# Kernel tuning notes

Measured on AMD Instinct MI355X. Metric: run time of the kernel, lower is better.

Reference implementation:

```python
import jax, jax.numpy as jnp
import numpy as np

N_USER, N_ITEM, N_BUNDLE = 200000, 100000, 50000
EMBED_DIM = 128
B, L = 8192, 100  # batch of bundles, max items per bundle


def setup_inputs() -> dict:
    key = jax.random.key(0)
    ks = jax.random.split(key, 12)
    d, d2 = EMBED_DIM, 2 * EMBED_DIM
    x_u = jax.random.randint(ks[0], (B,), 0, N_USER)
    x_b = jax.random.randint(ks[1], (B,), 0, N_BUNDLE)
    items = jax.random.randint(ks[2], (B, L), 0, N_ITEM)
    # ragged bundle sizes in [10, L]; padded+masked form of the CSR gather
    lengths = jax.random.randint(ks[3], (B,), 10, L + 1)
    mask = jnp.arange(L)[None, :] < lengths[:, None]  # [B, L] bool
    return {
        "x_u": x_u,
        "x_b": x_b,
        "items": items,
        "mask": mask,
        "emb_u": jax.random.normal(ks[4], (N_USER, d), jnp.float32) * 0.1,
        "emb_i": jax.random.normal(ks[5], (N_ITEM, d), jnp.float32) * 0.1,
        "emb_b": jax.random.normal(ks[6], (N_BUNDLE, d), jnp.float32) * 0.1,
        "A": jax.random.normal(ks[7], (N_ITEM, d), jnp.float32) * 0.1,
        "fc1_w": jax.random.normal(ks[8], (d2, d2), jnp.float32) / np.sqrt(d2),
        "fc1_b": jnp.zeros((d2,), jnp.float32),
        "fc2_w": jax.random.normal(ks[9], (d2, d2), jnp.float32) / np.sqrt(d2),
        "fc2_b": jnp.zeros((d2,), jnp.float32),
        "out_w": jax.random.normal(ks[10], (1, d2), jnp.float32) / np.sqrt(d2),
        "out_b": jnp.zeros((1,), jnp.float32),
    }


def reference(x_u, x_b, items, mask, emb_u, emb_i, emb_b, A,
              fc1_w, fc1_b, fc2_w, fc2_b, out_w, out_b):
    # DAM.forward_bundle with the attention() per-bundle loop vectorized
    h_u = emb_u[x_u]                       # [B, d]
    h_b = emb_b[x_b]                       # [B, d]
    item_e = emb_i[items]                  # [B, L, d] ragged gather (padded)
    a_e = A[items]                         # [B, L, d]
    # w = softmax_l( sum_d e_u * A[item] ) per bundle, over valid items only
    scores = jnp.einsum('bd,bld->bl', h_u, a_e)
    scores = jnp.where(mask, scores, -jnp.inf)
    w = jax.nn.softmax(scores, axis=1)     # [B, L]
    h_x = jnp.einsum('bl,bld->bd', w, item_e)
    h = jnp.concatenate([h_u, h_b + h_x], axis=1)   # [B, 2d]
    h = jax.nn.leaky_relu(h @ fc1_w.T + fc1_b)
    h = jax.nn.leaky_relu(h @ fc2_w.T + fc2_b)
    return h @ out_w.T + out_b             # [B, 1]
```

## Files before the change

### kernel.cpp

```cpp
#include <hip/hip_runtime.h>
#include <hip/hip_bf16.h>

#define D   128
#define D2  256
#define H1P 272

typedef short bf16x8 __attribute__((ext_vector_type(8)));
typedef float f32x4  __attribute__((ext_vector_type(4)));

__device__ __forceinline__ float bf2f(unsigned short u) {
    return __uint_as_float(((unsigned int)u) << 16);
}
__device__ __forceinline__ float bflo(unsigned int p) { return __uint_as_float(p << 16); }
__device__ __forceinline__ float bfhi(unsigned int p) { return __uint_as_float(p & 0xffff0000u); }
__device__ __forceinline__ unsigned short f2bf(float f) {
    __hip_bfloat16 h = __float2bfloat16(f);
    return *(unsigned short*)&h;
}

template<bool BF>
__device__ __forceinline__ float ld1(const void* p, size_t i) {
    if constexpr (BF) return bf2f(((const unsigned short*)p)[i]);
    else              return ((const float*)p)[i];
}

template<bool BF>
__device__ __forceinline__ void load8f(const void* p, size_t elem_off, float* r) {
    if constexpr (BF) {
        uint4 v = *(const uint4*)((const unsigned short*)p + elem_off);
        r[0]=bflo(v.x); r[1]=bfhi(v.x); r[2]=bflo(v.y); r[3]=bfhi(v.y);
        r[4]=bflo(v.z); r[5]=bfhi(v.z); r[6]=bflo(v.w); r[7]=bfhi(v.w);
    } else {
        const float4* q = (const float4*)((const float*)p + elem_off);
        float4 a = q[0], b = q[1];
        r[0]=a.x; r[1]=a.y; r[2]=a.z; r[3]=a.w;
        r[4]=b.x; r[5]=b.y; r[6]=b.z; r[7]=b.w;
    }
}

__device__ __forceinline__ bool probe_is_bf16(const unsigned int* probe) {
    const int lane = threadIdx.x & 63;
    int cnt = 0;
    #pragma unroll
    for (int i = 0; i < 4; ++i) {
        unsigned int e = (probe[lane + 64 * i] >> 7) & 0xffu;
        cnt += (e >= 90 && e < 130) ? 1 : 0;
    }
    #pragma unroll
    for (int o = 32; o; o >>= 1) cnt += __shfl_xor(cnt, o);
    return cnt >= 128;
}

template<bool BF>
__device__ __forceinline__ void attn_body(
    const int* __restrict__ x_u, const int* __restrict__ x_b,
    const int* __restrict__ items, const void* __restrict__ mask, int mmode,
    const void* __restrict__ emb_u, const void* __restrict__ emb_i,
    const void* __restrict__ emb_b, const void* __restrict__ Aw,
    unsigned short* __restrict__ h_out, int L,
    float* hu_s, float* w_s, int* it_s, int* cnt_s, float* reds_s,
    float (*part_s)[132])
{
    const int b  = blockIdx.x;
    const int t  = threadIdx.x;
    const int wv = t >> 6, ln = t & 63;

    const int xu = x_u[b], xb = x_b[b];
    float hu = 0.f;
    if (t < D) { hu = ld1<BF>(emb_u, (size_t)xu * D + t); hu_s[t] = hu; }

    bool valid = false;
    if (t < 128) {
        const int tc = (t < L) ? t : (L - 1);
        it_s[t] = items[(size_t)b * L + tc];
        if (t < L) {
            const size_t mi = (size_t)b * L + t;
            if (mmode == 0)      valid = ((const int*)mask)[mi] != 0;
            else if (mmode == 1) valid = ((const unsigned char*)mask)[mi] != 0;
            else                 valid = ((const unsigned short*)mask)[mi] != 0;
        }
    }
    unsigned long long bm = __ballot(valid);
    if (ln == 0) cnt_s[wv] = __popcll(bm);
    __syncthreads();
    const int len = cnt_s[0] + cnt_s[1] + cnt_s[2] + cnt_s[3];

    const int g = t >> 4, m16 = t & 15;

    uint4 pre0[3], pre1[3];
    if constexpr (BF) {
        const unsigned short* EI = (const unsigned short*)emb_i;
        #pragma unroll
        for (int i = 0; i < 3; ++i) {
            const int l0 = 32 * i + g, l1 = 32 * i + 16 + g;
            const int i0 = (l0 < len) ? it_s[l0] : it_s[0];
            const int i1 = (l1 < len) ? it_s[l1] : it_s[0];
            pre0[i] = *(const uint4*)(EI + (size_t)i0 * D + 8 * m16);
            pre1[i] = *(const uint4*)(EI + (size_t)i1 * D + 8 * m16);
        }
    }

    const int item = t >> 1, half = t & 1;
    float e = 0.f;
    if (item < len) {
        float acc = 0.f, r[8];
        const size_t base = (size_t)it_s[item] * D + half * 64;
        const float4* hu4 = (const float4*)hu_s + half * 16;
        #pragma unroll
        for (int c = 0; c < 8; ++c) {
            load8f<BF>(Aw, base + 8 * c, r);
            float4 ha = hu4[2 * c], hb2 = hu4[2 * c + 1];
            acc += ha.x * r[0] + ha.y * r[1] + ha.z * r[2] + ha.w * r[3]
                 + hb2.x * r[4] + hb2.y * r[5] + hb2.z * r[6] + hb2.w * r[7];
        }
        acc += __shfl_xor(acc, 1);
        e = __expf(acc);
    }
    if (half == 0) w_s[item] = e;
    float es = (half == 0) ? e : 0.f;
    #pragma unroll
    for (int o = 32; o; o >>= 1) es += __shfl_xor(es, o);
    if (ln == 0) reds_s[wv] = es;
    __syncthreads();
    const float sm  = reds_s[0] + reds_s[1] + reds_s[2] + reds_s[3];
    const float inv = (sm > 0.f) ? 1.f / sm : 0.f;

    float acc8[8];
    #pragma unroll
    for (int k = 0; k < 8; ++k) acc8[k] = 0.f;
    if constexpr (BF) {
        #pragma unroll
        for (int i = 0; i < 3; ++i) {
            const float w0 = w_s[32 * i + g], w1 = w_s[32 * i + 16 + g];
            const uint4 p0 = pre0[i], p1 = pre1[i];
            acc8[0] += w0 * bflo(p0.x) + w1 * bflo(p1.x);
            acc8[1] += w0 * bfhi(p0.x) + w1 * bfhi(p1.x);
            acc8[2] += w0 * bflo(p0.y) + w1 * bflo(p1.y);
            acc8[3] += w0 * bfhi(p0.y) + w1 * bfhi(p1.y);
            acc8[4] += w0 * bflo(p0.z) + w1 * bflo(p1.z);
            acc8[5] += w0 * bfhi(p0.z) + w1 * bfhi(p1.z);
            acc8[6] += w0 * bflo(p0.w) + w1 * bflo(p1.w);
            acc8[7] += w0 * bfhi(p0.w) + w1 * bfhi(p1.w);
        }
        if (len > 96) {
            const int l0 = 96 + g;
            const int i0 = (l0 < len) ? it_s[l0] : it_s[0];
            const float w0 = w_s[l0];
            const uint4 p0 = *(const uint4*)((const unsigned short*)emb_i
                                             + (size_t)i0 * D + 8 * m16);
            acc8[0] += w0 * bflo(p0.x); acc8[1] += w0 * bfhi(p0.x);
            acc8[2] += w0 * bflo(p0.y); acc8[3] += w0 * bfhi(p0.y);
            acc8[4] += w0 * bflo(p0.z); acc8[5] += w0 * bfhi(p0.z);
            acc8[6] += w0 * bflo(p0.w); acc8[7] += w0 * bfhi(p0.w);
        }
    } else {
        const int nit = (len + 31) & ~31;
        for (int i = 0; i < nit; i += 32) {
            const int l0 = i + g, l1 = i + 16 + g;
            const int i0 = (l0 < len) ? it_s[l0] : it_s[0];
            const int i1 = (l1 < len) ? it_s[l1] : it_s[0];
            const float w0 = w_s[l0], w1 = w_s[l1];
            float r0[8], r1[8];
            load8f<false>(emb_i, (size_t)i0 * D + 8 * m16, r0);
            load8f<false>(emb_i, (size_t)i1 * D + 8 * m16, r1);
            #pragma unroll
            for (int k = 0; k < 8; ++k) acc8[k] += w0 * r0[k] + w1 * r1[k];
        }
    }
    f32x4 v0 = {acc8[0] * inv, acc8[1] * inv, acc8[2] * inv, acc8[3] * inv};
    f32x4 v1 = {acc8[4] * inv, acc8[5] * inv, acc8[6] * inv, acc8[7] * inv};
    *(f32x4*)&part_s[g][8 * m16]     = v0;
    *(f32x4*)&part_s[g][8 * m16 + 4] = v1;
    __syncthreads();

    if (t < D) {
        float hx = 0.f;
        #pragma unroll
        for (int gg = 0; gg < 16; ++gg) hx += part_s[gg][t];
        const float hbv = ld1<BF>(emb_b, (size_t)xb * D + t);
        h_out[(size_t)b * D2 + t]     = f2bf(hu);
        h_out[(size_t)b * D2 + D + t] = f2bf(hbv + hx);
    }
}

__global__ __launch_bounds__(256) void attn_kernel(
    const int* x_u, const int* x_b, const int* items, const void* mask,
    const void* emb_u, const void* emb_i, const void* emb_b, const void* A,
    unsigned short* h_out, int L)
{
    __shared__ float hu_s[D];
    __shared__ float w_s[128];
    __shared__ int   it_s[128];
    __shared__ int   cnt_s[4];
    __shared__ float reds_s[4];
    __shared__ float part_s[16][132];

    const bool bf = probe_is_bf16((const unsigned int*)emb_u);
    const unsigned char* mb = (const unsigned char*)mask;
    const int mm = (mb[1] == 0) ? 0 : ((mb[0] == 1) ? 1 : 2);

    if (bf) attn_body<true >(x_u, x_b, items, mask, mm, emb_u, emb_i, emb_b, A,
                             h_out, L, hu_s, w_s, it_s, cnt_s, reds_s, part_s);
    else    attn_body<false>(x_u, x_b, items, mask, mm, emb_u, emb_i, emb_b, A,
                             h_out, L, hu_s, w_s, it_s, cnt_s, reds_s, part_s);
}

template<bool BF>
__device__ __forceinline__ bf16x8 load_w8(const void* W, size_t off) {
    if constexpr (BF) {
        return *(const bf16x8*)((const unsigned short*)W + off);
    } else {
        const float* p = (const float*)W + off;
        float4 a = *(const float4*)p;
        float4 b = *(const float4*)(p + 4);
        bf16x8 r;
        r[0] = (short)f2bf(a.x); r[1] = (short)f2bf(a.y);
        r[2] = (short)f2bf(a.z); r[3] = (short)f2bf(a.w);
        r[4] = (short)f2bf(b.x); r[5] = (short)f2bf(b.y);
        r[6] = (short)f2bf(b.z); r[7] = (short)f2bf(b.w);
        return r;
    }
}

template<bool BF>
__device__ __forceinline__ void mlp_body(
    const unsigned short* __restrict__ X,
    const void* __restrict__ fc1_w, const void* __restrict__ fc1_b,
    const void* __restrict__ fc2_w, const void* __restrict__ fc2_b,
    const void* __restrict__ out_w, const void* __restrict__ out_b,
    void* __restrict__ out,
    unsigned short* h1_s, float (*po_s)[16])
{
    const int tid  = threadIdx.x;
    const int wave = tid >> 6;
    const int lane = tid & 63;
    const int l16  = lane & 15;
    const int quad = lane >> 4;
    const int mt   = blockIdx.x * 16;

    bf16x8 afrag[8];
    const size_t abase = (size_t)(mt + l16) * D2 + quad * 8;
    #pragma unroll
    for (int kc = 0; kc < 8; ++kc)
        afrag[kc] = *(const bf16x8*)(X + abase + kc * 32);

    #pragma unroll
    for (int jj = 0; jj < 4; ++jj) {
        const int jt = wave * 4 + jj;
        const size_t bbase = (size_t)(jt * 16 + l16) * D2 + quad * 8;
        f32x4 acc = {0.f, 0.f, 0.f, 0.f};
        #pragma unroll
        for (int kc = 0; kc < 8; ++kc) {
            bf16x8 bfrag = load_w8<BF>(fc1_w, bbase + kc * 32);
            acc = __builtin_amdgcn_mfma_f32_16x16x32_bf16(afrag[kc], bfrag, acc, 0, 0, 0);
        }
        const int j  = jt * 16 + l16;
        const float bj = ld1<BF>(fc1_b, j);
        #pragma unroll
        for (int r = 0; r < 4; ++r) {
            float v = acc[r] + bj;
            v = v > 0.f ? v : 0.01f * v;
            h1_s[(quad * 4 + r) * H1P + j] = f2bf(v);
        }
    }
    __syncthreads();

    bf16x8 afrag2[8];
    #pragma unroll
    for (int kc = 0; kc < 8; ++kc)
        afrag2[kc] = *(const bf16x8*)&h1_s[l16 * H1P + quad * 8 + kc * 32];

    float po[4] = {0.f, 0.f, 0.f, 0.f};
    #pragma unroll
    for (int jj = 0; jj < 4; ++jj) {
        const int jt = wave * 4 + jj;
        const size_t bbase = (size_t)(jt * 16 + l16) * D2 + quad * 8;
        f32x4 acc = {0.f, 0.f, 0.f, 0.f};
        #pragma unroll
        for (int kc = 0; kc < 8; ++kc) {
            bf16x8 bfrag = load_w8<BF>(fc2_w, bbase + kc * 32);
            acc = __builtin_amdgcn_mfma_f32_16x16x32_bf16(afrag2[kc], bfrag, acc, 0, 0, 0);
        }
        const int j  = jt * 16 + l16;
        const float bj = ld1<BF>(fc2_b, j);
        const float wj = ld1<BF>(out_w, j);
        #pragma unroll
        for (int r = 0; r < 4; ++r) {
            float v = acc[r] + bj;
            v = v > 0.f ? v : 0.01f * v;
            po[r] += v * wj;
        }
    }
    #pragma unroll
    for (int r = 0; r < 4; ++r) {
        #pragma unroll
        for (int o = 1; o < 16; o <<= 1) po[r] += __shfl_xor(po[r], o);
    }
    if (l16 == 0) {
        #pragma unroll
        for (int r = 0; r < 4; ++r) po_s[wave][quad * 4 + r] = po[r];
    }
    __syncthreads();

    if (tid < 16) {
        const float v = po_s[0][tid] + po_s[1][tid] + po_s[2][tid] + po_s[3][tid]
                      + ld1<BF>(out_b, 0);
        if constexpr (BF) ((unsigned short*)out)[mt + tid] = f2bf(v);
        else              ((float*)out)[mt + tid] = v;
    }
}

__global__ __launch_bounds__(256) void mlp_kernel(
    const unsigned short* X,
    const void* fc1_w, const void* fc1_b, const void* fc2_w, const void* fc2_b,
    const void* out_w, const void* out_b, void* out, const void* probe)
{
    __shared__ unsigned short h1_s[16 * H1P];
    __shared__ float po_s[4][16];

    const bool bf = probe_is_bf16((const unsigned int*)probe);
    if (bf) mlp_body<true >(X, fc1_w, fc1_b, fc2_w, fc2_b, out_w, out_b, out, h1_s, po_s);
    else    mlp_body<false>(X, fc1_w, fc1_b, fc2_w, fc2_b, out_w, out_b, out, h1_s, po_s);
}

extern "C" void kernel_launch(void* const* d_in, const int* in_sizes, int n_in,
                              void* d_out, int out_size, void* d_ws, size_t ws_size,
                              hipStream_t stream) {
    const int*  x_u   = (const int*)d_in[0];
    const int*  x_b   = (const int*)d_in[1];
    const int*  items = (const int*)d_in[2];
    const void* mask  = d_in[3];
    const void* emb_u = d_in[4];
    const void* emb_i = d_in[5];
    const void* emb_b = d_in[6];
    const void* A     = d_in[7];
    const void* fc1_w = d_in[8];
    const void* fc1_b = d_in[9];
    const void* fc2_w = d_in[10];
    const void* fc2_b = d_in[11];
    const void* out_w = d_in[12];
    const void* out_b = d_in[13];

    const int B = in_sizes[0];
    const int L = in_sizes[2] / B;

    unsigned short* h = (unsigned short*)d_ws;

    attn_kernel<<<B, 256, 0, stream>>>(x_u, x_b, items, mask,
                                       emb_u, emb_i, emb_b, A, h, L);
    mlp_kernel<<<B / 16, 256, 0, stream>>>(h, fc1_w, fc1_b, fc2_w, fc2_b,
                                           out_w, out_b, d_out, emb_u);
}
```

Before: 320.7 us.

## Map one bundle per wavefront in attention kernel, replacing shared memory with shuffles

The attention kernel now assigns each bundle to a single 64-lane wavefront instead of a 256-thread block. Item ids, weights and partial sums move between lanes with shuffles instead of shared memory and __syncthreads. This removes block-level barriers and LDS traffic and lets each wave proceed on its own. In exchange, each wave issues all the gathers for its bundle serially, with less memory-level parallelism per bundle, and carries more register pressure (hu[32], e[7]). It also assumes L <= 128 and B divisible by 4.

```diff
diff --git a/kernel.cpp b/kernel.cpp
--- a/kernel.cpp
+++ b/kernel.cpp
@@ -38,6 +38,19 @@
     }
 }
 
+__device__ __forceinline__ void store8bf(unsigned short* p, const float* r) {
+    union { unsigned short u[8]; uint4 v; } pk;
+    #pragma unroll
+    for (int k = 0; k < 8; ++k) pk.u[k] = f2bf(r[k]);
+    *(uint4*)p = pk.v;
+}
+
+__device__ __forceinline__ bool read_mask(const void* mask, int mmode, size_t i) {
+    if (mmode == 0) return ((const int*)mask)[i] != 0;
+    if (mmode == 1) return ((const unsigned char*)mask)[i] != 0;
+    return ((const unsigned short*)mask)[i] != 0;
+}
+
 __device__ __forceinline__ bool probe_is_bf16(const unsigned int* probe) {
     const int lane = threadIdx.x & 63;
     int cnt = 0;
@@ -52,134 +65,103 @@
 }
 
 template<bool BF>
-__device__ __forceinline__ void attn_body(
+__device__ __forceinline__ void attn_wave(
     const int* __restrict__ x_u, const int* __restrict__ x_b,
     const int* __restrict__ items, const void* __restrict__ mask, int mmode,
     const void* __restrict__ emb_u, const void* __restrict__ emb_i,
     const void* __restrict__ emb_b, const void* __restrict__ Aw,
-    unsigned short* __restrict__ h_out, int L,
-    float* hu_s, float* w_s, int* it_s, int* cnt_s, float* reds_s,
-    float (*part_s)[132])
+    unsigned short* __restrict__ h_out, int L)
 {
-    const int b  = blockIdx.x;
-    const int t  = threadIdx.x;
-    const int wv = t >> 6, ln = t & 63;
+    const int lane = threadIdx.x & 63;
+    const int wv   = threadIdx.x >> 6;
+    const int b    = blockIdx.x * 4 + wv;
 
     const int xu = x_u[b], xb = x_b[b];
-    float hu = 0.f;
-    if (t < D) { hu = ld1<BF>(emb_u, (size_t)xu * D + t); hu_s[t] = hu; }
-
-    bool valid = false;
-    if (t < 128) {
-        const int tc = (t < L) ? t : (L - 1);
-        it_s[t] = items[(size_t)b * L + tc];
-        if (t < L) {
-            const size_t mi = (size_t)b * L + t;
-            if (mmode == 0)      valid = ((const int*)mask)[mi] != 0;
-            else if (mmode == 1) valid = ((const unsigned char*)mask)[mi] != 0;
-            else                 valid = ((const unsigned short*)mask)[mi] != 0;
-        }
-    }
-    unsigned long long bm = __ballot(valid);
-    if (ln == 0) cnt_s[wv] = __popcll(bm);
-    __syncthreads();
-    const int len = cnt_s[0] + cnt_s[1] + cnt_s[2] + cnt_s[3];
-
-    const int g = t >> 4, m16 = t & 15;
-
-    uint4 pre0[3], pre1[3];
-    if constexpr (BF) {
-        const unsigned short* EI = (const unsigned short*)emb_i;
-        #pragma unroll
-        for (int i = 0; i < 3; ++i) {
-            const int l0 = 32 * i + g, l1 = 32 * i + 16 + g;
-            const int i0 = (l0 < len) ? it_s[l0] : it_s[0];
-            const int i1 = (l1 < len) ? it_s[l1] : it_s[0];
-            pre0[i] = *(const uint4*)(EI + (size_t)i0 * D + 8 * m16);
-            pre1[i] = *(const uint4*)(EI + (size_t)i1 * D + 8 * m16);
-        }
-    }
-
-    const int item = t >> 1, half = t & 1;
-    float e = 0.f;
-    if (item < len) {
-        float acc = 0.f, r[8];
-        const size_t base = (size_t)it_s[item] * D + half * 64;
-        const float4* hu4 = (const float4*)hu_s + half * 16;
-        #pragma unroll
-        for (int c = 0; c < 8; ++c) {
-            load8f<BF>(Aw, base + 8 * c, r);
-            float4 ha = hu4[2 * c], hb2 = hu4[2 * c + 1];
-            acc += ha.x * r[0] + ha.y * r[1] + ha.z * r[2] + ha.w * r[3]
-                 + hb2.x * r[4] + hb2.y * r[5] + hb2.z * r[6] + hb2.w * r[7];
-        }
-        acc += __shfl_xor(acc, 1);
-        e = __expf(acc);
-    }
-    if (half == 0) w_s[item] = e;
-    float es = (half == 0) ? e : 0.f;
-    #pragma unroll
-    for (int o = 32; o; o >>= 1) es += __shfl_xor(es, o);
-    if (ln == 0) reds_s[wv] = es;
-    __syncthreads();
-    const float sm  = reds_s[0] + reds_s[1] + reds_s[2] + reds_s[3];
-    const float inv = (sm > 0.f) ? 1.f / sm : 0.f;
-
+
+    const int  c0 = (lane < L) ? lane : 0;
+    int  i0 = items[(size_t)b * L + c0];
+    bool v0 = (lane < L) && read_mask(mask, mmode, (size_t)b * L + c0);
+    int  i1 = i0;
+    bool v1 = false;
+    if (64 + lane < L) {
+        i1 = items[(size_t)b * L + 64 + lane];
+        v1 = read_mask(mask, mmode, (size_t)b * L + 64 + lane);
+    }
+    const int len = __popcll(__ballot(v0)) + __popcll(__ballot(v1));
+
+    const int seg = lane & 3;
+    float hu[32];
+    #pragma unroll
+    for (int j = 0; j < 4; ++j)
+        load8f<BF>(emb_u, (size_t)xu * D + seg * 32 + j * 8, hu + j * 8);
+
+    const int itm4 = lane >> 2;
+    float e[7];
+    float e_sum = 0.f;
+    #pragma unroll
+    for (int c = 0; c < 7; ++c) {
+        e[c] = 0.f;
+        if (c == 0 || c * 16 < len) {
+            const int i  = c * 16 + itm4;
+            const int id = (c < 4) ? __shfl(i0, i) : __shfl(i1, i - 64);
+            float acc = 0.f, r[8];
+            #pragma unroll
+            for (int j = 0; j < 4; ++j) {
+                load8f<BF>(Aw, (size_t)id * D + seg * 32 + j * 8, r);
+                #pragma unroll
+                for (int k = 0; k < 8; ++k) acc += hu[j * 8 + k] * r[k];
+            }
+            acc += __shfl_xor(acc, 1);
+            acc += __shfl_xor(acc, 2);
+            const float ev = (i < len) ? __expf(acc) : 0.f;
+            e[c] = ev;
+            if ((lane & 3) == 0) e_sum += ev;
+        }
+    }
+    #pragma unroll
+    for (int o = 32; o; o >>= 1) e_sum += __shfl_xor(e_sum, o);
+    const float inv = (e_sum > 0.f) ? 1.f / e_sum : 0.f;
+
+    const int g = lane >> 4, m16 = lane & 15;
     float acc8[8];
     #pragma unroll
     for (int k = 0; k < 8; ++k) acc8[k] = 0.f;
-    if constexpr (BF) {
-        #pragma unroll
-        for (int i = 0; i < 3; ++i) {
-            const float w0 = w_s[32 * i + g], w1 = w_s[32 * i + 16 + g];
-            const uint4 p0 = pre0[i], p1 = pre1[i];
-            acc8[0] += w0 * bflo(p0.x) + w1 * bflo(p1.x);
-            acc8[1] += w0 * bfhi(p0.x) + w1 * bfhi(p1.x);
-            acc8[2] += w0 * bflo(p0.y) + w1 * bflo(p1.y);
-            acc8[3] += w0 * bfhi(p0.y) + w1 * bfhi(p1.y);
-            acc8[4] += w0 * bflo(p0.z) + w1 * bflo(p1.z);
-            acc8[5] += w0 * bfhi(p0.z) + w1 * bfhi(p1.z);
-            acc8[6] += w0 * bflo(p0.w) + w1 * bflo(p1.w);
-            acc8[7] += w0 * bfhi(p0.w) + w1 * bfhi(p1.w);
-        }
-        if (len > 96) {
-            const int l0 = 96 + g;
-            const int i0 = (l0 < len) ? it_s[l0] : it_s[0];
-            const float w0 = w_s[l0];
-            const uint4 p0 = *(const uint4*)((const unsigned short*)emb_i
-                                             + (size_t)i0 * D + 8 * m16);
-            acc8[0] += w0 * bflo(p0.x); acc8[1] += w0 * bfhi(p0.x);
-            acc8[2] += w0 * bflo(p0.y); acc8[3] += w0 * bfhi(p0.y);
-            acc8[4] += w0 * bflo(p0.z); acc8[5] += w0 * bfhi(p0.z);
-            acc8[6] += w0 * bflo(p0.w); acc8[7] += w0 * bfhi(p0.w);
-        }
-    } else {
-        const int nit = (len + 31) & ~31;
-        for (int i = 0; i < nit; i += 32) {
-            const int l0 = i + g, l1 = i + 16 + g;
-            const int i0 = (l0 < len) ? it_s[l0] : it_s[0];
-            const int i1 = (l1 < len) ? it_s[l1] : it_s[0];
-            const float w0 = w_s[l0], w1 = w_s[l1];
-            float r0[8], r1[8];
-            load8f<false>(emb_i, (size_t)i0 * D + 8 * m16, r0);
-            load8f<false>(emb_i, (size_t)i1 * D + 8 * m16, r1);
+    #pragma unroll
+    for (int p = 0; p < 13; ++p) {
+        if (p == 0 || p * 8 < len) {
+            const int ia = p * 8 + g, ib = ia + 4;
+            const int ida = (p < 8) ? __shfl(i0, ia) : __shfl(i1, ia - 64);
+            const int idb = (p < 8) ? __shfl(i0, ib) : __shfl(i1, ib - 64);
+            const float wa = __shfl(e[p >> 1], (ia & 15) << 2);
+            const float wb = __shfl(e[p >> 1], (ib & 15) << 2);
+            float ra[8], rb[8];
+            load8f<BF>(emb_i, (size_t)ida * D + m16 * 8, ra);
+            load8f<BF>(emb_i, (size_t)idb * D + m16 * 8, rb);
             #pragma unroll
-            for (int k = 0; k < 8; ++k) acc8[k] += w0 * r0[k] + w1 * r1[k];
-        }
-    }
-    f32x4 v0 = {acc8[0] * inv, acc8[1] * inv, acc8[2] * inv, acc8[3] * inv};
-    f32x4 v1 = {acc8[4] * inv, acc8[5] * inv, acc8[6] * inv, acc8[7] * inv};
-    *(f32x4*)&part_s[g][8 * m16]     = v0;
-    *(f32x4*)&part_s[g][8 * m16 + 4] = v1;
-    __syncthreads();
-
-    if (t < D) {
-        float hx = 0.f;
-        #pragma unroll
-        for (int gg = 0; gg < 16; ++gg) hx += part_s[gg][t];
-        const float hbv = ld1<BF>(emb_b, (size_t)xb * D + t);
-        h_out[(size_t)b * D2 + t]     = f2bf(hu);
-        h_out[(size_t)b * D2 + D + t] = f2bf(hbv + hx);
+            for (int k = 0; k < 8; ++k) acc8[k] += wa * ra[k] + wb * rb[k];
+        }
+    }
+    #pragma unroll
+    for (int k = 0; k < 8; ++k) {
+        acc8[k] += __shfl_xor(acc8[k], 16);
+        acc8[k] += __shfl_xor(acc8[k], 32);
+    }
+
+    if (g == 0) {
+        if constexpr (BF) {
+            uint4 raw = *(const uint4*)((const unsigned short*)emb_u
+                                        + (size_t)xu * D + m16 * 8);
+            *(uint4*)(h_out + (size_t)b * D2 + m16 * 8) = raw;
+        } else {
+            float r[8];
+            load8f<false>(emb_u, (size_t)xu * D + m16 * 8, r);
+            store8bf(h_out + (size_t)b * D2 + m16 * 8, r);
+        }
+        float rb2[8], outv[8];
+        load8f<BF>(emb_b, (size_t)xb * D + m16 * 8, rb2);
+        #pragma unroll
+        for (int k = 0; k < 8; ++k) outv[k] = rb2[k] + acc8[k] * inv;
+        store8bf(h_out + (size_t)b * D2 + D + m16 * 8, outv);
     }
 }
 
@@ -188,21 +170,12 @@
     const void* emb_u, const void* emb_i, const void* emb_b, const void* A,
     unsigned short* h_out, int L)
 {
-    __shared__ float hu_s[D];
-    __shared__ float w_s[128];
-    __shared__ int   it_s[128];
-    __shared__ int   cnt_s[4];
-    __shared__ float reds_s[4];
-    __shared__ float part_s[16][132];
-
     const bool bf = probe_is_bf16((const unsigned int*)emb_u);
     const unsigned char* mb = (const unsigned char*)mask;
     const int mm = (mb[1] == 0) ? 0 : ((mb[0] == 1) ? 1 : 2);
 
-    if (bf) attn_body<true >(x_u, x_b, items, mask, mm, emb_u, emb_i, emb_b, A,
-                             h_out, L, hu_s, w_s, it_s, cnt_s, reds_s, part_s);
-    else    attn_body<false>(x_u, x_b, items, mask, mm, emb_u, emb_i, emb_b, A,
-                             h_out, L, hu_s, w_s, it_s, cnt_s, reds_s, part_s);
+    if (bf) attn_wave<true >(x_u, x_b, items, mask, mm, emb_u, emb_i, emb_b, A, h_out, L);
+    else    attn_wave<false>(x_u, x_b, items, mask, mm, emb_u, emb_i, emb_b, A, h_out, L);
 }
 
 template<bool BF>
@@ -346,8 +319,8 @@
 
     unsigned short* h = (unsigned short*)d_ws;
 
-    attn_kernel<<<B, 256, 0, stream>>>(x_u, x_b, items, mask,
-                                       emb_u, emb_i, emb_b, A, h, L);
+    attn_kernel<<<B / 4, 256, 0, stream>>>(x_u, x_b, items, mask,
+                                           emb_u, emb_i, emb_b, A, h, L);
     mlp_kernel<<<B / 16, 256, 0, stream>>>(h, fc1_w, fc1_b, fc2_w, fc2_b,
                                            out_w, out_b, d_out, emb_u);
 }
```

Measured after the change: 313.8 us. -2.2%, faster.
